# Kernel optimization log

Hardware: AMD Instinct MI355X
Metric: run time of the kernel (lower is better)

Reference implementation:

```python
import jax, jax.numpy as jnp
import numpy as np

K = 32  # neighbors per point (self.k)

def setup_inputs() -> dict:
    key = jax.random.key(0)
    k1, k2 = jax.random.split(key)
    B, N, C = 16, 4096, 64
    x = jax.random.normal(k1, (B, N, C), dtype=jnp.float32)
    idx = jax.random.randint(k2, (B, N, K), 0, N, dtype=jnp.int64)
    return {"x": x, "idx": idx}

def reference(x, idx):
    # pooled[b, n, :] = mean_k x[b, idx[b, n, k], :]
    # gather per-batch: xb[ib] -> [N, K, C]
    gathered = jax.vmap(lambda xb, ib: xb[ib])(x, idx)  # [B, N, K, C]
    return gathered.mean(axis=2)  # [B, N, C]
```

## Files before the change

kernel.cpp:

```cpp
#include <hip/hip_runtime.h>


#define BB 16
#define NN 4096
#define KK 32
#define CC 64
#define CH8 8
#define NCHUNK (CC / CH8)
#define NQ 4
#define PTS (NN / NQ)
#define THREADS 512
#define IDX16_ELEMS (BB * NN * KK)
#define PREP_BLOCKS 2048
#define PREP_THREADS 256

__device__ __forceinline__ uint pk_bf16(float a, float b) {
    uint ua = __float_as_uint(a);
    ua = (ua + 0x7fffu + ((ua >> 16) & 1u)) >> 16;
    uint ub = __float_as_uint(b);
    ub = (ub + 0x7fffu + ((ub >> 16) & 1u)) & 0xffff0000u;
    return ua | ub;
}

__global__ __launch_bounds__(PREP_THREADS)
void prep_kernel(const float* __restrict__ x,
                 const int* __restrict__ idx32,
                 ushort* __restrict__ idx16,
                 uint4* __restrict__ xbf) {
    int vprobe = idx32[2 * (threadIdx.x & 63) + 1];
    const int is64 = (__ballot(vprobe != 0) == 0ULL) ? 1 : 0;

    const int tid = blockIdx.x * blockDim.x + threadIdx.x;
    const int stride = gridDim.x * blockDim.x;

    if (is64) {
        const int4* __restrict__ in = (const int4*)idx32;
        uint* __restrict__ o = (uint*)idx16;
        for (int i = tid; i < IDX16_ELEMS / 2; i += stride) {
            int4 v = in[i];
            o[i] = (uint)(v.x & 0xFFFF) | ((uint)(v.z & 0xFFFF) << 16);
        }
    } else {
        const int4* __restrict__ in = (const int4*)idx32;
        uint2* __restrict__ o = (uint2*)idx16;
        for (int i = tid; i < IDX16_ELEMS / 4; i += stride) {
            int4 v = in[i];
            o[i] = make_uint2((uint)(v.x & 0xFFFF) | ((uint)(v.y & 0xFFFF) << 16),
                              (uint)(v.z & 0xFFFF) | ((uint)(v.w & 0xFFFF) << 16));
        }
    }

    {
        const int u = tid;
        const int row = u >> 3;
        const int ch = u & 7;
        const int b = row >> 12;
        const int n = row & (NN - 1);
        const float4* __restrict__ x4 = (const float4*)x;
        const float4 v0 = x4[(size_t)row * (CC / 4) + ch * 2];
        const float4 v1 = x4[(size_t)row * (CC / 4) + ch * 2 + 1];
        xbf[(size_t)(b * NCHUNK + ch) * NN + n] =
            make_uint4(pk_bf16(v0.x, v0.y), pk_bf16(v0.z, v0.w),
                       pk_bf16(v1.x, v1.y), pk_bf16(v1.z, v1.w));
    }
}

__device__ __forceinline__ void acc8(float a[8], uint4 r) {
    a[0] += __uint_as_float(r.x << 16);
    a[1] += __uint_as_float(r.x & 0xffff0000u);
    a[2] += __uint_as_float(r.y << 16);
    a[3] += __uint_as_float(r.y & 0xffff0000u);
    a[4] += __uint_as_float(r.z << 16);
    a[5] += __uint_as_float(r.z & 0xffff0000u);
    a[6] += __uint_as_float(r.w << 16);
    a[7] += __uint_as_float(r.w & 0xffff0000u);
}

__global__ __launch_bounds__(THREADS, 4)
void gapool_bf16_kernel(const ushort* __restrict__ idx16,
                        const uint4* __restrict__ xbf,
                        float* __restrict__ out) {
    __shared__ uint4 tile[NN];

    const int bid = blockIdx.x;
    const int b = bid & 15;
    const int g = bid >> 4;
    const int chunk = g & (NCHUNK - 1);
    const int q = g >> 3;
    const int tid = threadIdx.x;
    const float s = 1.0f / KK;

    const ushort* __restrict__ idxq =
        idx16 + ((size_t)b * NN + (size_t)q * PTS) * KK;
    float* __restrict__ outq =
        out + ((size_t)b * NN + (size_t)q * PTS) * CC + chunk * CH8;
    const uint4* __restrict__ src = xbf + (size_t)(b * NCHUNK + chunk) * NN;

    const uint4* __restrict__ ip0 = (const uint4*)(idxq + (size_t)tid * KK);
    uint4 pa = ip0[0], pb = ip0[1], pc = ip0[2], pd = ip0[3];

    for (int r = tid; r < NN; r += THREADS) tile[r] = src[r];
    __syncthreads();

    for (int p = tid; p < PTS; p += THREADS) {
        const uint w[16] = {pa.x, pa.y, pa.z, pa.w, pb.x, pb.y, pb.z, pb.w,
                            pc.x, pc.y, pc.z, pc.w, pd.x, pd.y, pd.z, pd.w};
        if (p + THREADS < PTS) {
            const uint4* ipn =
                (const uint4*)(idxq + (size_t)(p + THREADS) * KK);
            pa = ipn[0]; pb = ipn[1]; pc = ipn[2]; pd = ipn[3];
        }

        float a[8] = {0.f, 0.f, 0.f, 0.f, 0.f, 0.f, 0.f, 0.f};
#pragma unroll
        for (int i = 0; i < 16; ++i) {
            acc8(a, tile[w[i] & 0xFFFFu]);
            acc8(a, tile[w[i] >> 16]);
        }

        float4* op = (float4*)(outq + (size_t)p * CC);
        op[0] = make_float4(a[0] * s, a[1] * s, a[2] * s, a[3] * s);
        op[1] = make_float4(a[4] * s, a[5] * s, a[6] * s, a[7] * s);
    }
}

extern "C" void kernel_launch(void* const* d_in, const int* in_sizes, int n_in,
                              void* d_out, int out_size, void* d_ws, size_t ws_size,
                              hipStream_t stream) {
    const float* x     = (const float*)d_in[0];
    const int*   idx32 = (const int*)d_in[1];
    float*       out   = (float*)d_out;
    ushort*      idx16 = (ushort*)d_ws;
    uint4*       xbf   = (uint4*)((char*)d_ws + IDX16_ELEMS * 2);

    prep_kernel<<<PREP_BLOCKS, PREP_THREADS, 0, stream>>>(x, idx32, idx16, xbf);

    gapool_bf16_kernel<<<BB * NCHUNK * NQ, THREADS, 0, stream>>>(
        idx16, xbf, out);
}
```

Before: 87.22 us.

## Split gather-pool into LDS-tile blocks and direct fp32 global-gather blocks

The pooling kernel is restructured so each batch's points are divided between two block types. 256 blocks stage a bf16 channel chunk in shared memory and handle the last 3072 points in two halves, while 512 extra blocks gather the first 1024 points directly from the fp32 input through cache, one wavefront lane per channel. The goal is to cut the redundant per-block tile loads and balance shared-memory work against cache-served gathers. The trade-offs are lower occupancy (launch bounds drop to 2 blocks per SM), every block still reserving the 64KB shared tile including the global-path blocks, and a mix of fp32 and bf16-rounded results across different points.

```diff
diff --git a/kernel.cpp b/kernel.cpp
--- a/kernel.cpp
+++ b/kernel.cpp
@@ -7,12 +7,15 @@
 #define CC 64
 #define CH8 8
 #define NCHUNK (CC / CH8)
-#define NQ 4
-#define PTS (NN / NQ)
 #define THREADS 512
 #define IDX16_ELEMS (BB * NN * KK)
 #define PREP_BLOCKS 2048
 #define PREP_THREADS 256
+#define PL2 1024
+#define PLDS (NN - PL2)
+#define PHALF (PLDS / 2)
+#define LDS_BLOCKS (BB * NCHUNK * 2)
+#define L2_BLOCKS 512
 
 __device__ __forceinline__ uint pk_bf16(float a, float b) {
     uint ua = __float_as_uint(a);
@@ -76,51 +79,80 @@
     a[7] += __uint_as_float(r.w & 0xffff0000u);
 }
 
-__global__ __launch_bounds__(THREADS, 4)
-void gapool_bf16_kernel(const ushort* __restrict__ idx16,
+__global__ __launch_bounds__(THREADS, 2)
+void gapool_dual_kernel(const float* __restrict__ x,
+                        const ushort* __restrict__ idx16,
                         const uint4* __restrict__ xbf,
                         float* __restrict__ out) {
     __shared__ uint4 tile[NN];
 
     const int bid = blockIdx.x;
     const int b = bid & 15;
-    const int g = bid >> 4;
-    const int chunk = g & (NCHUNK - 1);
-    const int q = g >> 3;
     const int tid = threadIdx.x;
     const float s = 1.0f / KK;
 
-    const ushort* __restrict__ idxq =
-        idx16 + ((size_t)b * NN + (size_t)q * PTS) * KK;
-    float* __restrict__ outq =
-        out + ((size_t)b * NN + (size_t)q * PTS) * CC + chunk * CH8;
-    const uint4* __restrict__ src = xbf + (size_t)(b * NCHUNK + chunk) * NN;
+    if (bid < LDS_BLOCKS) {
+        const int g = bid >> 4;
+        const int chunk = g & (NCHUNK - 1);
+        const int half = g >> 3;
+        const int n0 = PL2 + half * PHALF;
 
-    const uint4* __restrict__ ip0 = (const uint4*)(idxq + (size_t)tid * KK);
-    uint4 pa = ip0[0], pb = ip0[1], pc = ip0[2], pd = ip0[3];
+        const ushort* __restrict__ idxq =
+            idx16 + ((size_t)b * NN + n0) * KK;
+        float* __restrict__ outq =
+            out + ((size_t)b * NN + n0) * CC + chunk * CH8;
+        const uint4* __restrict__ src = xbf + (size_t)(b * NCHUNK + chunk) * NN;
 
-    for (int r = tid; r < NN; r += THREADS) tile[r] = src[r];
-    __syncthreads();
+        const uint4* __restrict__ ip0 = (const uint4*)(idxq + (size_t)tid * KK);
+        uint4 pa = ip0[0], pb = ip0[1], pc = ip0[2], pd = ip0[3];
 
-    for (int p = tid; p < PTS; p += THREADS) {
-        const uint w[16] = {pa.x, pa.y, pa.z, pa.w, pb.x, pb.y, pb.z, pb.w,
-                            pc.x, pc.y, pc.z, pc.w, pd.x, pd.y, pd.z, pd.w};
-        if (p + THREADS < PTS) {
-            const uint4* ipn =
-                (const uint4*)(idxq + (size_t)(p + THREADS) * KK);
-            pa = ipn[0]; pb = ipn[1]; pc = ipn[2]; pd = ipn[3];
+        for (int r = tid; r < NN; r += THREADS) tile[r] = src[r];
+        __syncthreads();
+
+        for (int p = tid; p < PHALF; p += THREADS) {
+            const uint w[16] = {pa.x, pa.y, pa.z, pa.w, pb.x, pb.y, pb.z, pb.w,
+                                pc.x, pc.y, pc.z, pc.w, pd.x, pd.y, pd.z, pd.w};
+            if (p + THREADS < PHALF) {
+                const uint4* ipn =
+                    (const uint4*)(idxq + (size_t)(p + THREADS) * KK);
+                pa = ipn[0]; pb = ipn[1]; pc = ipn[2]; pd = ipn[3];
+            }
+
+            float a[8] = {0.f, 0.f, 0.f, 0.f, 0.f, 0.f, 0.f, 0.f};
+#pragma unroll
+            for (int i = 0; i < 16; ++i) {
+                acc8(a, tile[w[i] & 0xFFFFu]);
+                acc8(a, tile[w[i] >> 16]);
+            }
+
+            float4* op = (float4*)(outq + (size_t)p * CC);
+            op[0] = make_float4(a[0] * s, a[1] * s, a[2] * s, a[3] * s);
+            op[1] = make_float4(a[4] * s, a[5] * s, a[6] * s, a[7] * s);
         }
+    } else {
+        const int t = bid - LDS_BLOCKS;
+        const int grp = t >> 4;
+        const int wv = __builtin_amdgcn_readfirstlane(tid >> 6);
+        const int lane = tid & 63;
 
-        float a[8] = {0.f, 0.f, 0.f, 0.f, 0.f, 0.f, 0.f, 0.f};
+        const float* __restrict__ xb = x + (size_t)b * NN * CC;
+        float* __restrict__ outb = out + (size_t)b * NN * CC;
+        const ushort* __restrict__ idxb = idx16 + (size_t)b * NN * KK;
+
 #pragma unroll
-        for (int i = 0; i < 16; ++i) {
-            acc8(a, tile[w[i] & 0xFFFFu]);
-            acc8(a, tile[w[i] >> 16]);
+        for (int tt = 0; tt < 4; ++tt) {
+            const int n = grp * 32 + wv * 4 + tt;
+            const uint* __restrict__ ip =
+                (const uint*)(idxb + (size_t)n * KK);
+            float acc = 0.f;
+#pragma unroll
+            for (int i = 0; i < 16; ++i) {
+                const uint w = ip[i];
+                acc += xb[((w & 0xFFFFu) << 6) + lane];
+                acc += xb[((w >> 16) << 6) + lane];
+            }
+            outb[(size_t)n * CC + lane] = acc * s;
         }
-
-        float4* op = (float4*)(outq + (size_t)p * CC);
-        op[0] = make_float4(a[0] * s, a[1] * s, a[2] * s, a[3] * s);
-        op[1] = make_float4(a[4] * s, a[5] * s, a[6] * s, a[7] * s);
     }
 }
 
@@ -135,6 +167,6 @@
 
     prep_kernel<<<PREP_BLOCKS, PREP_THREADS, 0, stream>>>(x, idx32, idx16, xbf);
 
-    gapool_bf16_kernel<<<BB * NCHUNK * NQ, THREADS, 0, stream>>>(
-        idx16, xbf, out);
+    gapool_dual_kernel<<<LDS_BLOCKS + L2_BLOCKS, THREADS, 0, stream>>>(
+        x, idx16, xbf, out);
 }
```

Measured after the change: 91.97 us. 5.4% more time.
